# Optimization experiments

Hardware: AMD Instinct MI355X
Metric: run time of the kernel (lower is better)

## Reference

```python
import jax, jax.numpy as jnp
import numpy as np

EMBED_D = 128
HID = EMBED_D // 2          # bi-LSTM hidden per direction
GENE_N = 200000
CELL_N = 100000
BATCH = 200000
TRIPLE_INDEX = 1            # gene-cell triples


def setup_inputs() -> dict:
    key = jax.random.key(0)
    ks = jax.random.split(key, 16)
    s = 1.0 / np.sqrt(HID)  # torch LSTM init scale
    inp = {
        # embedding tables (feature_list[0]=gene, feature_list[1]=cell)
        "gene_feat": jax.random.normal(ks[0], (GENE_N, EMBED_D), jnp.float32),
        "cell_feat": jax.random.normal(ks[1], (CELL_N, EMBED_D), jnp.float32),
        # gene_content_rnn: forward & reverse input weights and (b_ih+b_hh) biases
        "gene_Wf": jax.random.uniform(ks[2], (4 * HID, EMBED_D), jnp.float32, -s, s),
        "gene_bf": jax.random.uniform(ks[3], (4 * HID,), jnp.float32, -s, s),
        "gene_Wb": jax.random.uniform(ks[4], (4 * HID, EMBED_D), jnp.float32, -s, s),
        "gene_bb": jax.random.uniform(ks[5], (4 * HID,), jnp.float32, -s, s),
        # cell_content_rnn
        "cell_Wf": jax.random.uniform(ks[6], (4 * HID, EMBED_D), jnp.float32, -s, s),
        "cell_bf": jax.random.uniform(ks[7], (4 * HID,), jnp.float32, -s, s),
        "cell_Wb": jax.random.uniform(ks[8], (4 * HID, EMBED_D), jnp.float32, -s, s),
        "cell_bb": jax.random.uniform(ks[9], (4 * HID,), jnp.float32, -s, s),
        # triple ids: center = gene (local==global); pos/neg = cells (global = local + GENE_n)
        "c_ids": jax.random.randint(ks[10], (BATCH,), 0, GENE_N, jnp.int64) if jax.config.jax_enable_x64 else jax.random.randint(ks[10], (BATCH,), 0, GENE_N, jnp.int32),
        "p_ids": jax.random.randint(ks[11], (BATCH,), 0, CELL_N, jnp.int32) + GENE_N,
        "n_ids": jax.random.randint(ks[12], (BATCH,), 0, CELL_N, jnp.int32) + GENE_N,
        "triple_index": TRIPLE_INDEX,
    }
    return inp


def _lstm1_bi(x, Wf, bf, Wb, bb):
    """Single-step bidirectional LSTM with zero initial state.
    x: [B, E]. With seq_len==1 both directions see the same single input and
    the recurrent weights contribute nothing (h0=c0=0), so:
      gates = x @ W_ih^T + (b_ih + b_hh); c = sigma(i)*tanh(g); h = sigma(o)*tanh(c).
    Gate order (torch): i, f, g, o. Output = concat(h_fwd, h_bwd) -> [B, E].
    """
    def step(W, b):
        g = x @ W.T + b                        # [B, 4H]
        i, f, gg, o = jnp.split(g, 4, axis=-1)
        c = jax.nn.sigmoid(i) * jnp.tanh(gg)   # f*c0 = 0
        return jax.nn.sigmoid(o) * jnp.tanh(c)
    return jnp.concatenate([step(Wf, bf), step(Wb, bb)], axis=-1)


def reference(gene_feat, cell_feat,
              gene_Wf, gene_bf, gene_Wb, gene_bb,
              cell_Wf, cell_bf, cell_Wb, cell_bb,
              c_ids, p_ids, n_ids, triple_index):
    assert triple_index == 1  # gene-cell triples
    # content_agg: gather -> seq_len=1 bi-LSTM -> mean over seq dim (identity for len 1)
    c_out = _lstm1_bi(gene_feat[c_ids], gene_Wf, gene_bf, gene_Wb, gene_bb)
    p_out = _lstm1_bi(cell_feat[p_ids - GENE_N], cell_Wf, cell_bf, cell_Wb, cell_bb)
    n_out = _lstm1_bi(cell_feat[n_ids - GENE_N], cell_Wf, cell_bf, cell_Wb, cell_bb)
    return c_out, p_out, n_out
```

## Files before the change

### kernel.cpp

```cpp
#include <hip/hip_runtime.h>

#define GENE_N  200000
#define BATCH   200000
#define EMBED   128
#define BM      32
#define THREADS 512
#define LDS_STRIDE 136
#define L2E     1.44269504088896340736f

typedef __attribute__((ext_vector_type(8))) short bf16x8;
typedef __attribute__((ext_vector_type(4))) float f32x4;

static __device__ __forceinline__ short f2bf(float f) {
    unsigned u = __builtin_bit_cast(unsigned, f);
    unsigned r = (u + 0x7fffu + ((u >> 16) & 1u)) >> 16;
    return (short)(r & 0xffffu);
}
static __device__ __forceinline__ unsigned cvt_pk_bf16(float lo, float hi) {
    unsigned r;
    asm("v_cvt_pk_bf16_f32 %0, %1, %2" : "=v"(r) : "v"(lo), "v"(hi));
    return r;
}

__global__ __launch_bounds__(THREADS, 4)
void hetagg_kernel(const float* __restrict__ gene_feat,
                   const float* __restrict__ cell_feat,
                   const float* __restrict__ gWf, const float* __restrict__ gbf,
                   const float* __restrict__ gWb, const float* __restrict__ gbb,
                   const float* __restrict__ cWf, const float* __restrict__ cbf,
                   const float* __restrict__ cWb, const float* __restrict__ cbb,
                   const int* __restrict__ c_ids, const int* __restrict__ p_ids,
                   const int* __restrict__ n_ids, float* __restrict__ out,
                   int gene_blocks, int cell_blocks)
{
    __shared__ short A_lds[2][BM * LDS_STRIDE];

    const int  bid     = blockIdx.x;
    const bool is_gene = (bid < gene_blocks);
    const int  tid     = threadIdx.x;
    const int  wid     = tid >> 6;
    const int  lane    = tid & 63;
    const int  lgrp    = lane >> 4;
    const int  lcol    = lane & 15;
    const int  dir     = wid >> 2;
    const int  jt      = wid & 3;
    const int  j       = jt * 16 + lcol;

    const float* feat = is_gene ? gene_feat : cell_feat;
    const float* W    = is_gene ? (dir ? gWb : gWf) : (dir ? cWb : cWf);
    const float* Bv   = is_gene ? (dir ? gbb : gbf) : (dir ? cbb : cbf);

    const float gsc[3] = {-L2E, 2.0f * L2E, -L2E};
    const float b0 = -L2E * Bv[j];
    const float b1 = 2.0f * L2E * Bv[128 + j];
    const float b2 = -L2E * Bv[192 + j];

    bf16x8 bfrag[3][4];
    {
        const int gate_base[3] = {0, 128, 192};
#pragma unroll
        for (int q = 0; q < 3; ++q) {
            const float* wrow = W + (size_t)(gate_base[q] + j) * EMBED;
            const float  sc   = gsc[q];
#pragma unroll
            for (int s = 0; s < 4; ++s) {
                const int k0 = s * 32 + lgrp * 8;
                float4 w0 = *(const float4*)(wrow + k0);
                float4 w1 = *(const float4*)(wrow + k0 + 4);
                bf16x8 b;
                b[0] = f2bf(sc * w0.x); b[1] = f2bf(sc * w0.y);
                b[2] = f2bf(sc * w0.z); b[3] = f2bf(sc * w0.w);
                b[4] = f2bf(sc * w1.x); b[5] = f2bf(sc * w1.y);
                b[6] = f2bf(sc * w1.z); b[7] = f2bf(sc * w1.w);
                bfrag[q][s] = b;
            }
        }
    }

    const int myb    = is_gene ? bid : (bid - gene_blocks);
    const int nb     = is_gene ? gene_blocks : cell_blocks;
    const int ntiles = is_gene ? (BATCH / BM) : (2 * BATCH / BM);
    const int nk     = (ntiles - myb + nb - 1) / nb;

    const int r0 = tid >> 5;
    const int cc = tid & 31;

#define FETCH_ID(grow) (is_gene ? c_ids[(grow)] \
                       : ((grow) < BATCH ? p_ids[(grow)] - GENE_N \
                                         : n_ids[(grow) - BATCH] - GENE_N))

    float4 rvA[2], rvB[2];
    int    idC[2];
    {
        int id0[2], id1[2];
        const int ta = myb * BM;
#pragma unroll
        for (int p = 0; p < 2; ++p) id0[p] = FETCH_ID(ta + r0 + p * 16);
#pragma unroll
        for (int p = 0; p < 2; ++p)
            rvA[p] = ((const float4*)(feat + (size_t)id0[p] * EMBED))[cc];
        if (nk > 1) {
            const int tb = (myb + nb) * BM;
#pragma unroll
            for (int p = 0; p < 2; ++p) id1[p] = FETCH_ID(tb + r0 + p * 16);
#pragma unroll
            for (int p = 0; p < 2; ++p)
                rvB[p] = ((const float4*)(feat + (size_t)id1[p] * EMBED))[cc];
        }
        if (nk > 2) {
            const int tc = (myb + 2 * nb) * BM;
#pragma unroll
            for (int p = 0; p < 2; ++p) idC[p] = FETCH_ID(tc + r0 + p * 16);
        }
    }

    int pb = 0;

#define TILE_BODY(K, RV)                                                        \
    {                                                                           \
        const int t_    = myb + (K) * nb;                                       \
        const int base_ = t_ * BM;                                              \
        short* buf = A_lds[pb];                                                 \
        _Pragma("unroll")                                                       \
        for (int p = 0; p < 2; ++p) {                                           \
            int2 sv;                                                            \
            sv.x = (int)cvt_pk_bf16(RV[p].x, RV[p].y);                          \
            sv.y = (int)cvt_pk_bf16(RV[p].z, RV[p].w);                          \
            *(int2*)&buf[(r0 + p * 16) * LDS_STRIDE + cc * 4] = sv;             \
        }                                                                       \
        asm volatile("s_waitcnt lgkmcnt(0)" ::: "memory");                      \
        __builtin_amdgcn_s_barrier();                                           \
        if ((K) + 2 < nk) {                                                     \
            _Pragma("unroll")                                                   \
            for (int p = 0; p < 2; ++p)                                         \
                RV[p] = ((const float4*)(feat + (size_t)idC[p] * EMBED))[cc];   \
        }                                                                       \
        if ((K) + 3 < nk) {                                                     \
            const int tn_ = (myb + ((K) + 3) * nb) * BM;                        \
            _Pragma("unroll")                                                   \
            for (int p = 0; p < 2; ++p) idC[p] = FETCH_ID(tn_ + r0 + p * 16);   \
        }                                                                       \
        _Pragma("unroll")                                                       \
        for (int mt = 0; mt < 2; ++mt) {                                        \
            f32x4 acc0 = {b0, b0, b0, b0};                                      \
            f32x4 acc1 = {b1, b1, b1, b1};                                      \
            f32x4 acc2 = {b2, b2, b2, b2};                                      \
            const int m_ = mt * 16 + lcol;                                      \
            _Pragma("unroll")                                                   \
            for (int s = 0; s < 4; ++s) {                                       \
                bf16x8 a = *(const bf16x8*)&buf[m_ * LDS_STRIDE + s * 32 + lgrp * 8]; \
                acc0 = __builtin_amdgcn_mfma_f32_16x16x32_bf16(a, bfrag[0][s], acc0, 0, 0, 0); \
                acc1 = __builtin_amdgcn_mfma_f32_16x16x32_bf16(a, bfrag[1][s], acc1, 0, 0, 0); \
                acc2 = __builtin_amdgcn_mfma_f32_16x16x32_bf16(a, bfrag[2][s], acc2, 0, 0, 0); \
            }                                                                   \
            _Pragma("unroll")                                                   \
            for (int r = 0; r < 4; ++r) {                                       \
                const float a0 = acc0[r];                                       \
                const float a1 = fminf(acc1[r], 80.0f);                         \
                const float a2 = acc2[r];                                       \
                const float u  = __builtin_amdgcn_exp2f(a0);                    \
                const float v  = __builtin_amdgcn_exp2f(a1);                    \
                const float w  = __builtin_amdgcn_exp2f(a2);                    \
                const float tprod = (1.0f + u) * (v + 1.0f);                    \
                const float c  = (v - 1.0f) * __builtin_amdgcn_rcpf(tprod);     \
                const float c2 = c * c;                                         \
                const float num = c * (15.0f + c2);                             \
                const float den = (15.0f + 6.0f * c2) * (1.0f + w);             \
                const float h   = num * __builtin_amdgcn_rcpf(den);             \
                const int row   = base_ + mt * 16 + lgrp * 4 + r;               \
                const size_t orow = (size_t)(is_gene ? row : (BATCH + row));    \
                out[orow * 128 + dir * 64 + j] = h;                             \
            }                                                                   \
        }                                                                       \
        pb ^= 1;                                                                \
    }

    int k = 0;
    for (; k + 1 < nk; k += 2) {
        TILE_BODY(k, rvA);
        TILE_BODY(k + 1, rvB);
    }
    if (k < nk) TILE_BODY(k, rvA);

#undef TILE_BODY
#undef FETCH_ID
}

extern "C" void kernel_launch(void* const* d_in, const int* in_sizes, int n_in,
                              void* d_out, int out_size, void* d_ws, size_t ws_size,
                              hipStream_t stream)
{
    const float* gene_feat = (const float*)d_in[0];
    const float* cell_feat = (const float*)d_in[1];
    const float* gWf = (const float*)d_in[2];
    const float* gbf = (const float*)d_in[3];
    const float* gWb = (const float*)d_in[4];
    const float* gbb = (const float*)d_in[5];
    const float* cWf = (const float*)d_in[6];
    const float* cbf = (const float*)d_in[7];
    const float* cWb = (const float*)d_in[8];
    const float* cbb = (const float*)d_in[9];
    const int* c_ids = (const int*)d_in[10];
    const int* p_ids = (const int*)d_in[11];
    const int* n_ids = (const int*)d_in[12];
    float* out = (float*)d_out;

    const int gene_blocks = 171;
    const int cell_blocks = 341;
    dim3 grid(gene_blocks + cell_blocks);
    dim3 block(THREADS);
    hipLaunchKernelGGL(hetagg_kernel, grid, block, 0, stream,
                       gene_feat, cell_feat, gWf, gbf, gWb, gbb,
                       cWf, cbf, cWb, cbb, c_ids, p_ids, n_ids, out,
                       gene_blocks, cell_blocks);
}
```

Baseline: 153.7 us.

## Process tile pairs per barrier and XOR-swizzle LDS instead of padding

Restructures the main loop so two tiles are staged into LDS together and share one barrier, with the gathers and id fetches for the next two tiles issued before computing both. The padded LDS stride is replaced by an XOR swizzle on 8-element groups to avoid bank conflicts without padding. This halves barrier count and deepens the prefetch, at the cost of more LDS (four buffers) and more live registers, which could reduce occupancy.

```diff
diff --git a/kernel.cpp b/kernel.cpp
--- a/kernel.cpp
+++ b/kernel.cpp
@@ -5,7 +5,6 @@
 #define EMBED   128
 #define BM      32
 #define THREADS 512
-#define LDS_STRIDE 136
 #define L2E     1.44269504088896340736f
 
 typedef __attribute__((ext_vector_type(8))) short bf16x8;
@@ -33,7 +32,7 @@
                    const int* __restrict__ n_ids, float* __restrict__ out,
                    int gene_blocks, int cell_blocks)
 {
-    __shared__ short A_lds[2][BM * LDS_STRIDE];
+    __shared__ short A_lds[2][2][BM * EMBED];
 
     const int  bid     = blockIdx.x;
     const bool is_gene = (bid < gene_blocks);
@@ -82,64 +81,54 @@
     const int ntiles = is_gene ? (BATCH / BM) : (2 * BATCH / BM);
     const int nk     = (ntiles - myb + nb - 1) / nb;
 
-    const int r0 = tid >> 5;
-    const int cc = tid & 31;
+    const int r0  = tid >> 5;
+    const int cc  = tid & 31;
+    const int wsw = (r0 & 7) << 3;
+    const int rsw = (lcol & 7) << 3;
 
 #define FETCH_ID(grow) (is_gene ? c_ids[(grow)] \
                        : ((grow) < BATCH ? p_ids[(grow)] - GENE_N \
                                          : n_ids[(grow) - BATCH] - GENE_N))
 
     float4 rvA[2], rvB[2];
-    int    idC[2];
+    int    idA[2], idB[2];
     {
         int id0[2], id1[2];
-        const int ta = myb * BM;
-#pragma unroll
-        for (int p = 0; p < 2; ++p) id0[p] = FETCH_ID(ta + r0 + p * 16);
+#pragma unroll
+        for (int p = 0; p < 2; ++p) id0[p] = FETCH_ID(myb * BM + r0 + p * 16);
 #pragma unroll
         for (int p = 0; p < 2; ++p)
             rvA[p] = ((const float4*)(feat + (size_t)id0[p] * EMBED))[cc];
         if (nk > 1) {
-            const int tb = (myb + nb) * BM;
-#pragma unroll
-            for (int p = 0; p < 2; ++p) id1[p] = FETCH_ID(tb + r0 + p * 16);
+#pragma unroll
+            for (int p = 0; p < 2; ++p) id1[p] = FETCH_ID((myb + nb) * BM + r0 + p * 16);
 #pragma unroll
             for (int p = 0; p < 2; ++p)
                 rvB[p] = ((const float4*)(feat + (size_t)id1[p] * EMBED))[cc];
         }
         if (nk > 2) {
-            const int tc = (myb + 2 * nb) * BM;
-#pragma unroll
-            for (int p = 0; p < 2; ++p) idC[p] = FETCH_ID(tc + r0 + p * 16);
-        }
-    }
-
-    int pb = 0;
-
-#define TILE_BODY(K, RV)                                                        \
+#pragma unroll
+            for (int p = 0; p < 2; ++p) idA[p] = FETCH_ID((myb + 2 * nb) * BM + r0 + p * 16);
+        }
+        if (nk > 3) {
+#pragma unroll
+            for (int p = 0; p < 2; ++p) idB[p] = FETCH_ID((myb + 3 * nb) * BM + r0 + p * 16);
+        }
+    }
+
+#define STAGE(RV, BUF)                                                          \
     {                                                                           \
-        const int t_    = myb + (K) * nb;                                       \
-        const int base_ = t_ * BM;                                              \
-        short* buf = A_lds[pb];                                                 \
         _Pragma("unroll")                                                       \
         for (int p = 0; p < 2; ++p) {                                           \
             int2 sv;                                                            \
             sv.x = (int)cvt_pk_bf16(RV[p].x, RV[p].y);                          \
             sv.y = (int)cvt_pk_bf16(RV[p].z, RV[p].w);                          \
-            *(int2*)&buf[(r0 + p * 16) * LDS_STRIDE + cc * 4] = sv;             \
+            *(int2*)&(BUF)[(r0 + p * 16) * EMBED + ((cc * 4) ^ wsw)] = sv;      \
         }                                                                       \
-        asm volatile("s_waitcnt lgkmcnt(0)" ::: "memory");                      \
-        __builtin_amdgcn_s_barrier();                                           \
-        if ((K) + 2 < nk) {                                                     \
-            _Pragma("unroll")                                                   \
-            for (int p = 0; p < 2; ++p)                                         \
-                RV[p] = ((const float4*)(feat + (size_t)idC[p] * EMBED))[cc];   \
-        }                                                                       \
-        if ((K) + 3 < nk) {                                                     \
-            const int tn_ = (myb + ((K) + 3) * nb) * BM;                        \
-            _Pragma("unroll")                                                   \
-            for (int p = 0; p < 2; ++p) idC[p] = FETCH_ID(tn_ + r0 + p * 16);   \
-        }                                                                       \
+    }
+
+#define TILE_COMPUTE(BASE, BUF)                                                 \
+    {                                                                           \
         _Pragma("unroll")                                                       \
         for (int mt = 0; mt < 2; ++mt) {                                        \
             f32x4 acc0 = {b0, b0, b0, b0};                                      \
@@ -148,7 +137,7 @@
             const int m_ = mt * 16 + lcol;                                      \
             _Pragma("unroll")                                                   \
             for (int s = 0; s < 4; ++s) {                                       \
-                bf16x8 a = *(const bf16x8*)&buf[m_ * LDS_STRIDE + s * 32 + lgrp * 8]; \
+                bf16x8 a = *(const bf16x8*)&(BUF)[m_ * EMBED + ((s * 32 + lgrp * 8) ^ rsw)]; \
                 acc0 = __builtin_amdgcn_mfma_f32_16x16x32_bf16(a, bfrag[0][s], acc0, 0, 0, 0); \
                 acc1 = __builtin_amdgcn_mfma_f32_16x16x32_bf16(a, bfrag[1][s], acc1, 0, 0, 0); \
                 acc2 = __builtin_amdgcn_mfma_f32_16x16x32_bf16(a, bfrag[2][s], acc2, 0, 0, 0); \
@@ -167,22 +156,58 @@
                 const float num = c * (15.0f + c2);                             \
                 const float den = (15.0f + 6.0f * c2) * (1.0f + w);             \
                 const float h   = num * __builtin_amdgcn_rcpf(den);             \
-                const int row   = base_ + mt * 16 + lgrp * 4 + r;               \
+                const int row   = (BASE) + mt * 16 + lgrp * 4 + r;              \
                 const size_t orow = (size_t)(is_gene ? row : (BATCH + row));    \
                 out[orow * 128 + dir * 64 + j] = h;                             \
             }                                                                   \
         }                                                                       \
-        pb ^= 1;                                                                \
-    }
-
-    int k = 0;
-    for (; k + 1 < nk; k += 2) {
-        TILE_BODY(k, rvA);
-        TILE_BODY(k + 1, rvB);
-    }
-    if (k < nk) TILE_BODY(k, rvA);
-
-#undef TILE_BODY
+    }
+
+    int pp = 0;
+    int k  = 0;
+    for (; k + 1 < nk; k += 2, pp ^= 1) {
+        short* buf0 = A_lds[pp][0];
+        short* buf1 = A_lds[pp][1];
+
+        STAGE(rvA, buf0);
+        STAGE(rvB, buf1);
+        asm volatile("s_waitcnt lgkmcnt(0)" ::: "memory");
+        __builtin_amdgcn_s_barrier();
+
+        if (k + 2 < nk) {
+#pragma unroll
+            for (int p = 0; p < 2; ++p)
+                rvA[p] = ((const float4*)(feat + (size_t)idA[p] * EMBED))[cc];
+        }
+        if (k + 3 < nk) {
+#pragma unroll
+            for (int p = 0; p < 2; ++p)
+                rvB[p] = ((const float4*)(feat + (size_t)idB[p] * EMBED))[cc];
+        }
+        if (k + 4 < nk) {
+            const int t4 = (myb + (k + 4) * nb) * BM;
+#pragma unroll
+            for (int p = 0; p < 2; ++p) idA[p] = FETCH_ID(t4 + r0 + p * 16);
+        }
+        if (k + 5 < nk) {
+            const int t5 = (myb + (k + 5) * nb) * BM;
+#pragma unroll
+            for (int p = 0; p < 2; ++p) idB[p] = FETCH_ID(t5 + r0 + p * 16);
+        }
+
+        TILE_COMPUTE((myb + k * nb) * BM, buf0);
+        TILE_COMPUTE((myb + (k + 1) * nb) * BM, buf1);
+    }
+    if (k < nk) {
+        short* buf0 = A_lds[pp][0];
+        STAGE(rvA, buf0);
+        asm volatile("s_waitcnt lgkmcnt(0)" ::: "memory");
+        __builtin_amdgcn_s_barrier();
+        TILE_COMPUTE((myb + k * nb) * BM, buf0);
+    }
+
+#undef TILE_COMPUTE
+#undef STAGE
 #undef FETCH_ID
 }
 
```

After: 161.0 us. 1.05x slower.

## Load A fragments directly from global memory, dropping LDS staging and barriers

Applied to the files above, without the earlier changes.

Each wave now reads its MFMA A-operand rows straight from the gathered embedding rows in global memory and converts them to bf16 in registers. This removes the shared-memory double buffer, the per-tile block barrier, and the software register prefetch of feature rows. The catch is that all 8 waves of a block re-read the same 32 rows, so global/L2 traffic per tile goes up about eightfold, and there is no explicit prefetch to hide gather latency beyond the lookahead on the id loads.

```diff
diff --git a/kernel.cpp b/kernel.cpp
--- a/kernel.cpp
+++ b/kernel.cpp
@@ -5,7 +5,6 @@
 #define EMBED   128
 #define BM      32
 #define THREADS 512
-#define LDS_STRIDE 136
 #define L2E     1.44269504088896340736f
 
 typedef __attribute__((ext_vector_type(8))) short bf16x8;
@@ -33,8 +32,6 @@
                    const int* __restrict__ n_ids, float* __restrict__ out,
                    int gene_blocks, int cell_blocks)
 {
-    __shared__ short A_lds[2][BM * LDS_STRIDE];
-
     const int  bid     = blockIdx.x;
     const bool is_gene = (bid < gene_blocks);
     const int  tid     = threadIdx.x;
@@ -82,107 +79,73 @@
     const int ntiles = is_gene ? (BATCH / BM) : (2 * BATCH / BM);
     const int nk     = (ntiles - myb + nb - 1) / nb;
 
-    const int r0 = tid >> 5;
-    const int cc = tid & 31;
-
 #define FETCH_ID(grow) (is_gene ? c_ids[(grow)] \
                        : ((grow) < BATCH ? p_ids[(grow)] - GENE_N \
                                          : n_ids[(grow) - BATCH] - GENE_N))
 
-    float4 rvA[2], rvB[2];
-    int    idC[2];
-    {
-        int id0[2], id1[2];
-        const int ta = myb * BM;
+    int idc[2], idn[2];
 #pragma unroll
-        for (int p = 0; p < 2; ++p) id0[p] = FETCH_ID(ta + r0 + p * 16);
+    for (int p = 0; p < 2; ++p) idc[p] = FETCH_ID(myb * BM + p * 16 + lcol);
 #pragma unroll
-        for (int p = 0; p < 2; ++p)
-            rvA[p] = ((const float4*)(feat + (size_t)id0[p] * EMBED))[cc];
-        if (nk > 1) {
-            const int tb = (myb + nb) * BM;
-#pragma unroll
-            for (int p = 0; p < 2; ++p) id1[p] = FETCH_ID(tb + r0 + p * 16);
-#pragma unroll
-            for (int p = 0; p < 2; ++p)
-                rvB[p] = ((const float4*)(feat + (size_t)id1[p] * EMBED))[cc];
-        }
-        if (nk > 2) {
-            const int tc = (myb + 2 * nb) * BM;
-#pragma unroll
-            for (int p = 0; p < 2; ++p) idC[p] = FETCH_ID(tc + r0 + p * 16);
-        }
+    for (int p = 0; p < 2; ++p)
+        idn[p] = (nk > 1) ? FETCH_ID((myb + nb) * BM + p * 16 + lcol) : 0;
+
+#define TILE_MT(RP, MT, BASE)                                                   \
+    {                                                                           \
+        f32x4 acc0 = {b0, b0, b0, b0};                                          \
+        f32x4 acc1 = {b1, b1, b1, b1};                                          \
+        f32x4 acc2 = {b2, b2, b2, b2};                                          \
+        const f32x4* rv4 = (const f32x4*)(RP);                                  \
+        _Pragma("unroll")                                                       \
+        for (int s = 0; s < 4; ++s) {                                           \
+            f32x4 lo = rv4[s * 8 + lgrp * 2];                                   \
+            f32x4 hi = rv4[s * 8 + lgrp * 2 + 1];                               \
+            int4 pk;                                                            \
+            pk.x = (int)cvt_pk_bf16(lo[0], lo[1]);                              \
+            pk.y = (int)cvt_pk_bf16(lo[2], lo[3]);                              \
+            pk.z = (int)cvt_pk_bf16(hi[0], hi[1]);                              \
+            pk.w = (int)cvt_pk_bf16(hi[2], hi[3]);                              \
+            bf16x8 a = __builtin_bit_cast(bf16x8, pk);                          \
+            acc0 = __builtin_amdgcn_mfma_f32_16x16x32_bf16(a, bfrag[0][s], acc0, 0, 0, 0); \
+            acc1 = __builtin_amdgcn_mfma_f32_16x16x32_bf16(a, bfrag[1][s], acc1, 0, 0, 0); \
+            acc2 = __builtin_amdgcn_mfma_f32_16x16x32_bf16(a, bfrag[2][s], acc2, 0, 0, 0); \
+        }                                                                       \
+        _Pragma("unroll")                                                       \
+        for (int r = 0; r < 4; ++r) {                                           \
+            const float a0 = acc0[r];                                           \
+            const float a1 = fminf(acc1[r], 80.0f);                             \
+            const float a2 = acc2[r];                                           \
+            const float u  = __builtin_amdgcn_exp2f(a0);                        \
+            const float v  = __builtin_amdgcn_exp2f(a1);                        \
+            const float w  = __builtin_amdgcn_exp2f(a2);                        \
+            const float tprod = (1.0f + u) * (v + 1.0f);                        \
+            const float c  = (v - 1.0f) * __builtin_amdgcn_rcpf(tprod);         \
+            const float c2 = c * c;                                             \
+            const float num = c * (15.0f + c2);                                 \
+            const float den = (15.0f + 6.0f * c2) * (1.0f + w);                 \
+            const float h   = num * __builtin_amdgcn_rcpf(den);                 \
+            const int row   = (BASE) + (MT) * 16 + lgrp * 4 + r;                \
+            const size_t orow = (size_t)(is_gene ? row : (BATCH + row));        \
+            out[orow * 128 + dir * 64 + j] = h;                                 \
+        }                                                                       \
     }
 
-    int pb = 0;
+    for (int k = 0; k < nk; ++k) {
+        const int base = (myb + k * nb) * BM;
+        const float* rp0 = feat + (size_t)idc[0] * EMBED;
+        const float* rp1 = feat + (size_t)idc[1] * EMBED;
+        idc[0] = idn[0]; idc[1] = idn[1];
+        if (k + 2 < nk) {
+            const int tb = (myb + (k + 2) * nb) * BM;
+#pragma unroll
+            for (int p = 0; p < 2; ++p) idn[p] = FETCH_ID(tb + p * 16 + lcol);
+        }
 
-#define TILE_BODY(K, RV)                                                        \
-    {                                                                           \
-        const int t_    = myb + (K) * nb;                                       \
-        const int base_ = t_ * BM;                                              \
-        short* buf = A_lds[pb];                                                 \
-        _Pragma("unroll")                                                       \
-        for (int p = 0; p < 2; ++p) {                                           \
-            int2 sv;                                                            \
-            sv.x = (int)cvt_pk_bf16(RV[p].x, RV[p].y);                          \
-            sv.y = (int)cvt_pk_bf16(RV[p].z, RV[p].w);                          \
-            *(int2*)&buf[(r0 + p * 16) * LDS_STRIDE + cc * 4] = sv;             \
-        }                                                                       \
-        asm volatile("s_waitcnt lgkmcnt(0)" ::: "memory");                      \
-        __builtin_amdgcn_s_barrier();                                           \
-        if ((K) + 2 < nk) {                                                     \
-            _Pragma("unroll")                                                   \
-            for (int p = 0; p < 2; ++p)                                         \
-                RV[p] = ((const float4*)(feat + (size_t)idC[p] * EMBED))[cc];   \
-        }                                                                       \
-        if ((K) + 3 < nk) {                                                     \
-            const int tn_ = (myb + ((K) + 3) * nb) * BM;                        \
-            _Pragma("unroll")                                                   \
-            for (int p = 0; p < 2; ++p) idC[p] = FETCH_ID(tn_ + r0 + p * 16);   \
-        }                                                                       \
-        _Pragma("unroll")                                                       \
-        for (int mt = 0; mt < 2; ++mt) {                                        \
-            f32x4 acc0 = {b0, b0, b0, b0};                                      \
-            f32x4 acc1 = {b1, b1, b1, b1};                                      \
-            f32x4 acc2 = {b2, b2, b2, b2};                                      \
-            const int m_ = mt * 16 + lcol;                                      \
-            _Pragma("unroll")                                                   \
-            for (int s = 0; s < 4; ++s) {                                       \
-                bf16x8 a = *(const bf16x8*)&buf[m_ * LDS_STRIDE + s * 32 + lgrp * 8]; \
-                acc0 = __builtin_amdgcn_mfma_f32_16x16x32_bf16(a, bfrag[0][s], acc0, 0, 0, 0); \
-                acc1 = __builtin_amdgcn_mfma_f32_16x16x32_bf16(a, bfrag[1][s], acc1, 0, 0, 0); \
-                acc2 = __builtin_amdgcn_mfma_f32_16x16x32_bf16(a, bfrag[2][s], acc2, 0, 0, 0); \
-            }                                                                   \
-            _Pragma("unroll")                                                   \
-            for (int r = 0; r < 4; ++r) {                                       \
-                const float a0 = acc0[r];                                       \
-                const float a1 = fminf(acc1[r], 80.0f);                         \
-                const float a2 = acc2[r];                                       \
-                const float u  = __builtin_amdgcn_exp2f(a0);                    \
-                const float v  = __builtin_amdgcn_exp2f(a1);                    \
-                const float w  = __builtin_amdgcn_exp2f(a2);                    \
-                const float tprod = (1.0f + u) * (v + 1.0f);                    \
-                const float c  = (v - 1.0f) * __builtin_amdgcn_rcpf(tprod);     \
-                const float c2 = c * c;                                         \
-                const float num = c * (15.0f + c2);                             \
-                const float den = (15.0f + 6.0f * c2) * (1.0f + w);             \
-                const float h   = num * __builtin_amdgcn_rcpf(den);             \
-                const int row   = base_ + mt * 16 + lgrp * 4 + r;               \
-                const size_t orow = (size_t)(is_gene ? row : (BATCH + row));    \
-                out[orow * 128 + dir * 64 + j] = h;                             \
-            }                                                                   \
-        }                                                                       \
-        pb ^= 1;                                                                \
+        TILE_MT(rp0, 0, base);
+        TILE_MT(rp1, 1, base);
     }
 
-    int k = 0;
-    for (; k + 1 < nk; k += 2) {
-        TILE_BODY(k, rvA);
-        TILE_BODY(k + 1, rvB);
-    }
-    if (k < nk) TILE_BODY(k, rvA);
-
-#undef TILE_BODY
+#undef TILE_MT
 #undef FETCH_ID
 }
 
```

Measured after the change: 310.4 us. 102% more time.

## Swap MFMA operands for vectorized float4 output stores and reorder prefetch

Applied to the files above, without the earlier changes.

Swaps the A and B operands of the MFMA so each lane's four accumulator values lie along the hidden dimension rather than the batch dimension. This lets each lane write one float4 per tile instead of four scattered scalar stores, and bias init becomes a per-lane vector. The global prefetch of the next rows is moved ahead of the LDS wait and barrier so it issues earlier. The gate math now uses a single reciprocal with all inputs clamped to 15, which trades some range and precision for fewer rcp instructions.

```diff
diff --git a/kernel.cpp b/kernel.cpp
--- a/kernel.cpp
+++ b/kernel.cpp
@@ -51,9 +51,15 @@
     const float* Bv   = is_gene ? (dir ? gbb : gbf) : (dir ? cbb : cbf);
 
     const float gsc[3] = {-L2E, 2.0f * L2E, -L2E};
-    const float b0 = -L2E * Bv[j];
-    const float b1 = 2.0f * L2E * Bv[128 + j];
-    const float b2 = -L2E * Bv[192 + j];
+
+    f32x4 binit0, binit1, binit2;
+#pragma unroll
+    for (int r = 0; r < 4; ++r) {
+        const int jr = jt * 16 + lgrp * 4 + r;
+        binit0[r] = -L2E * Bv[jr];
+        binit1[r] = 2.0f * L2E * Bv[128 + jr];
+        binit2[r] = -L2E * Bv[192 + jr];
+    }
 
     bf16x8 bfrag[3][4];
     {
@@ -128,49 +134,57 @@
             sv.y = (int)cvt_pk_bf16(RV[p].z, RV[p].w);                          \
             *(int2*)&buf[(r0 + p * 16) * LDS_STRIDE + cc * 4] = sv;             \
         }                                                                       \
+           \
+        if ((K) + 2 < nk) {                                                     \
+            _Pragma("unroll")                                                   \
+            for (int p = 0; p < 2; ++p)                                         \
+                RV[p] = ((const float4*)(feat + (size_t)idC[p] * EMBED))[cc];   \
+        }                                                                       \
+        if ((K) + 3 < nk) {                                                     \
+            const int tn_ = (myb + ((K) + 3) * nb) * BM;                        \
+            _Pragma("unroll")                                                   \
+            for (int p = 0; p < 2; ++p) idC[p] = FETCH_ID(tn_ + r0 + p * 16);   \
+        }                                                                       \
         asm volatile("s_waitcnt lgkmcnt(0)" ::: "memory");                      \
         __builtin_amdgcn_s_barrier();                                           \
-        if ((K) + 2 < nk) {                                                     \
-            _Pragma("unroll")                                                   \
-            for (int p = 0; p < 2; ++p)                                         \
-                RV[p] = ((const float4*)(feat + (size_t)idC[p] * EMBED))[cc];   \
-        }                                                                       \
-        if ((K) + 3 < nk) {                                                     \
-            const int tn_ = (myb + ((K) + 3) * nb) * BM;                        \
-            _Pragma("unroll")                                                   \
-            for (int p = 0; p < 2; ++p) idC[p] = FETCH_ID(tn_ + r0 + p * 16);   \
-        }                                                                       \
         _Pragma("unroll")                                                       \
         for (int mt = 0; mt < 2; ++mt) {                                        \
-            f32x4 acc0 = {b0, b0, b0, b0};                                      \
-            f32x4 acc1 = {b1, b1, b1, b1};                                      \
-            f32x4 acc2 = {b2, b2, b2, b2};                                      \
+            f32x4 acc0 = binit0;                                                \
+            f32x4 acc1 = binit1;                                                \
+            f32x4 acc2 = binit2;                                                \
             const int m_ = mt * 16 + lcol;                                      \
             _Pragma("unroll")                                                   \
             for (int s = 0; s < 4; ++s) {                                       \
                 bf16x8 a = *(const bf16x8*)&buf[m_ * LDS_STRIDE + s * 32 + lgrp * 8]; \
-                acc0 = __builtin_amdgcn_mfma_f32_16x16x32_bf16(a, bfrag[0][s], acc0, 0, 0, 0); \
-                acc1 = __builtin_amdgcn_mfma_f32_16x16x32_bf16(a, bfrag[1][s], acc1, 0, 0, 0); \
-                acc2 = __builtin_amdgcn_mfma_f32_16x16x32_bf16(a, bfrag[2][s], acc2, 0, 0, 0); \
+                acc0 = __builtin_amdgcn_mfma_f32_16x16x32_bf16(bfrag[0][s], a, acc0, 0, 0, 0); \
+                acc1 = __builtin_amdgcn_mfma_f32_16x16x32_bf16(bfrag[1][s], a, acc1, 0, 0, 0); \
+                acc2 = __builtin_amdgcn_mfma_f32_16x16x32_bf16(bfrag[2][s], a, acc2, 0, 0, 0); \
             }                                                                   \
+                  \
+                  \
+            float4 hv;                                                          \
             _Pragma("unroll")                                                   \
             for (int r = 0; r < 4; ++r) {                                       \
-                const float a0 = acc0[r];                                       \
-                const float a1 = fminf(acc1[r], 80.0f);                         \
-                const float a2 = acc2[r];                                       \
+                const float a0 = fminf(acc0[r], 15.0f);                         \
+                const float a1 = fminf(acc1[r], 15.0f);                         \
+                const float a2 = fminf(acc2[r], 15.0f);                         \
                 const float u  = __builtin_amdgcn_exp2f(a0);                    \
                 const float v  = __builtin_amdgcn_exp2f(a1);                    \
                 const float w  = __builtin_amdgcn_exp2f(a2);                    \
-                const float tprod = (1.0f + u) * (v + 1.0f);                    \
-                const float c  = (v - 1.0f) * __builtin_amdgcn_rcpf(tprod);     \
-                const float c2 = c * c;                                         \
-                const float num = c * (15.0f + c2);                             \
-                const float den = (15.0f + 6.0f * c2) * (1.0f + w);             \
-                const float h   = num * __builtin_amdgcn_rcpf(den);             \
-                const int row   = base_ + mt * 16 + lgrp * 4 + r;               \
-                const size_t orow = (size_t)(is_gene ? row : (BATCH + row));    \
-                out[orow * 128 + dir * 64 + j] = h;                             \
+                const float N  = v - 1.0f;                                      \
+                const float D  = (1.0f + u) * (v + 1.0f);                       \
+                const float D2 = D * D;                                         \
+                const float N2 = N * N;                                         \
+                const float t1 = fmaf(15.0f, D2, N2);                           \
+                const float t2 = fmaf(5.0f, N2, t1);                            \
+                const float num = N * t1;                                       \
+                const float den = D * t2 * (1.0f + w);                          \
+                hv[r] = num * __builtin_amdgcn_rcpf(den);                       \
             }                                                                   \
+            const int row = base_ + mt * 16 + lcol;                             \
+            const size_t orow = (size_t)(is_gene ? row : (BATCH + row));        \
+            *(float4*)&out[orow * 128 + dir * 64 + jt * 16 + lgrp * 4] =        \
+                *(const float4*)&hv;                                            \
         }                                                                       \
         pb ^= 1;                                                                \
     }
```

After: 168.5 us. 9.6% more time.
